# Optimization experiments

Measured on AMD Instinct MI355X. Metric: run time of the kernel, lower is better.

## Reference

```python
import jax, jax.numpy as jnp
import numpy as np

B, S, E, H = 32, 256, 768, 32
D = E // H  # head_dim = 24


def setup_inputs() -> dict:
    key = jax.random.key(0)
    ks = jax.random.split(key, 10)
    w_sc = 1.0 / np.sqrt(E)  # xavier-ish init scale for weights
    return {
        "feats": jax.random.normal(ks[0], (B, S, E), jnp.float32),
        "attn_bias": jax.random.normal(ks[1], (B, H, S, S), jnp.float32),
        "delta_pos": jax.random.normal(ks[2], (B, S, S, 3), jnp.float32),
        "Wq": jax.random.normal(ks[3], (E, E), jnp.float32) * w_sc,
        "bq": jnp.zeros((E,), jnp.float32),
        "Wk": jax.random.normal(ks[4], (E, E), jnp.float32) * w_sc,
        "bk": jnp.zeros((E,), jnp.float32),
        "Wv": jax.random.normal(ks[5], (E, E), jnp.float32) * w_sc,
        "bv": jnp.zeros((E,), jnp.float32),
        "Wfx": jax.random.normal(ks[6], (E,), jnp.float32) * w_sc,
        "Wfy": jax.random.normal(ks[7], (E,), jnp.float32) * w_sc,
        "Wfz": jax.random.normal(ks[8], (E,), jnp.float32) * w_sc,
    }


def reference(feats, attn_bias, delta_pos, Wq, bq, Wk, bk, Wv, bv, Wfx, Wfy, Wfz):
    b, s, e = feats.shape
    h = attn_bias.shape[1]
    d = e // h
    scaling = d ** -0.5
    # q/k/v projections; q scaled by 1/sqrt(head_dim)
    q = ((feats @ Wq + bq) * scaling).reshape(b, s, h, d).transpose(0, 2, 1, 3)  # (b,h,s,d)
    k = (feats @ Wk + bk).reshape(b, s, h, d).transpose(0, 2, 1, 3)              # (b,h,t,d)
    v = (feats @ Wv + bv).reshape(b, s, h, d).transpose(0, 2, 1, 3)              # (b,h,t,d)
    scores = jnp.einsum('bhsd,bhtd->bhst', q, k) + attn_bias
    probs = jax.nn.softmax(scores, axis=-1)  # dropout p in eval -> identity
    # rot_attn_probs = probs[...,None] * delta_pos[:,None] fused into one contraction:
    # (b,h,s,t) * (b,s,t,3) contracted with (b,h,t,c) over t -> (b,s,3,h,c)
    attn = jnp.einsum('bhst,bstx,bhtc->bsxhc', probs, delta_pos, v)
    attn = attn.reshape(b, s, 3, e)  # flatten (h,c) -> e
    out_x = attn[..., 0, :] @ Wfx  # (b,s)
    out_y = attn[..., 1, :] @ Wfy
    out_z = attn[..., 2, :] @ Wfz
    return jnp.stack([out_x, out_y, out_z], axis=-1)  # (b,s,3)
```

## Files before the change

### kernel.cpp

```cpp
#include <hip/hip_runtime.h>
#include <hip/hip_bf16.h>

#define B_ 32
#define S_ 256
#define E_ 768
#define H_ 32
#define D_ 24
#define NTOT 1664
#define LK 40

typedef __hip_bfloat16 bf16;
typedef __attribute__((ext_vector_type(8))) short short8;
typedef __attribute__((ext_vector_type(4))) float floatx4;

__global__ __launch_bounds__(256) void cast_feats(
    const float* __restrict__ in, bf16* __restrict__ outp, int n4)
{
  int i = blockIdx.x * 256 + threadIdx.x;
  if (i < n4) {
    float4 v = reinterpret_cast<const float4*>(in)[i];
    union { ushort4 u; bf16 b[4]; } pk;
    pk.b[0] = (bf16)v.x; pk.b[1] = (bf16)v.y;
    pk.b[2] = (bf16)v.z; pk.b[3] = (bf16)v.w;
    reinterpret_cast<ushort4*>(outp)[i] = pk.u;
  }
}

__global__ __launch_bounds__(256) void prep_pack(
    const float* __restrict__ Wq, const float* __restrict__ Wk,
    const float* __restrict__ Wv,
    const float* __restrict__ bq, const float* __restrict__ bk,
    const float* __restrict__ bv,
    const float* __restrict__ Wfx, const float* __restrict__ Wfy,
    const float* __restrict__ Wfz,
    bf16* __restrict__ Wt, float* __restrict__ biasf)
{
  const float qscale = 0.20412414523193154f;
  int gid = blockIdx.x * 256 + threadIdx.x;
  if (gid < NTOT * E_) {
    int n = gid / E_, k = gid % E_;
    float val;
    if (n < 768) {
      val = Wq[(size_t)k * E_ + n] * qscale;
    } else if (n < 1536) {
      val = Wk[(size_t)k * E_ + (n - 768)];
    } else if (n < 1632) {
      int nn = n - 1536, x = nn >> 5, h = nn & 31;
      const float* Wf = (x == 0) ? Wfx : (x == 1 ? Wfy : Wfz);
      float s = 0.f;
      #pragma unroll
      for (int c = 0; c < D_; c++)
        s += Wv[(size_t)k * E_ + h * D_ + c] * Wf[h * D_ + c];
      val = s;
    } else {
      val = 0.f;
    }
    Wt[gid] = (bf16)val;
  } else {
    int n = gid - NTOT * E_;
    if (n < NTOT) {
      float val;
      if (n < 768) {
        val = bq[n] * qscale;
      } else if (n < 1536) {
        val = bk[n - 768];
      } else if (n < 1632) {
        int nn = n - 1536, x = nn >> 5, h = nn & 31;
        const float* Wf = (x == 0) ? Wfx : (x == 1 ? Wfy : Wfz);
        float s = 0.f;
        #pragma unroll
        for (int c = 0; c < D_; c++)
          s += bv[h * D_ + c] * Wf[h * D_ + c];
        val = s;
      } else {
        val = 0.f;
      }
      biasf[n] = val;
    }
  }
}

__global__ __launch_bounds__(256) void gemm_qkv(
    const bf16* __restrict__ A, const bf16* __restrict__ Wt,
    const float* __restrict__ biasf,
    bf16* __restrict__ qout, bf16* __restrict__ kout,
    float* __restrict__ vwout)
{
  __shared__ __align__(16) short As[128 * LK];
  __shared__ __align__(16) short Bs[128 * LK];
  int tid = threadIdx.x;
  int m0 = blockIdx.y * 128, n0 = blockIdx.x * 128;
  int lrow = tid >> 2, lcol = (tid & 3) * 8;
  int wave = tid >> 6, lane = tid & 63;
  int wm = (wave >> 1) * 64, wn = (wave & 1) * 64;
  int fr = lane & 15, quad = lane >> 4;

  floatx4 acc[4][4];
  const floatx4 zero = {0.f, 0.f, 0.f, 0.f};
  #pragma unroll
  for (int i = 0; i < 4; i++)
    #pragma unroll
    for (int j = 0; j < 4; j++) acc[i][j] = zero;

  for (int k0 = 0; k0 < E_; k0 += 32) {
    float4 av0 = *reinterpret_cast<const float4*>(
        A + (size_t)(m0 + lrow) * E_ + k0 + lcol);
    float4 av1 = *reinterpret_cast<const float4*>(
        A + (size_t)(m0 + 64 + lrow) * E_ + k0 + lcol);
    float4 bv0 = *reinterpret_cast<const float4*>(
        Wt + (size_t)(n0 + lrow) * E_ + k0 + lcol);
    float4 bv1 = *reinterpret_cast<const float4*>(
        Wt + (size_t)(n0 + 64 + lrow) * E_ + k0 + lcol);
    __syncthreads();
    *reinterpret_cast<float4*>(&As[lrow * LK + lcol]) = av0;
    *reinterpret_cast<float4*>(&As[(lrow + 64) * LK + lcol]) = av1;
    *reinterpret_cast<float4*>(&Bs[lrow * LK + lcol]) = bv0;
    *reinterpret_cast<float4*>(&Bs[(lrow + 64) * LK + lcol]) = bv1;
    __syncthreads();
    short8 af[4], bfr[4];
    #pragma unroll
    for (int t = 0; t < 4; t++)
      af[t] = *reinterpret_cast<const short8*>(
          &As[(wm + t * 16 + fr) * LK + quad * 8]);
    #pragma unroll
    for (int t = 0; t < 4; t++)
      bfr[t] = *reinterpret_cast<const short8*>(
          &Bs[(wn + t * 16 + fr) * LK + quad * 8]);
    #pragma unroll
    for (int ti = 0; ti < 4; ti++)
      #pragma unroll
      for (int tj = 0; tj < 4; tj++)
        acc[ti][tj] = __builtin_amdgcn_mfma_f32_16x16x32_bf16(
            af[ti], bfr[tj], acc[ti][tj], 0, 0, 0);
  }

  #pragma unroll
  for (int ti = 0; ti < 4; ti++) {
    #pragma unroll
    for (int tj = 0; tj < 4; tj++) {
      int n = n0 + wn + tj * 16 + fr;
      float bias = biasf[n];
      #pragma unroll
      for (int r = 0; r < 4; r++) {
        int m = m0 + wm + ti * 16 + quad * 4 + r;
        int b = m >> 8, s = m & 255;
        float val = acc[ti][tj][r] + bias;
        if (n < 768) {
          int h = n / 24, d = n - h * 24;
          qout[(((size_t)b * H_ + h) * S_ + s) * D_ + d] = (bf16)val;
        } else if (n < 1536) {
          int n2 = n - 768;
          int h = n2 / 24, d = n2 - h * 24;
          kout[(((size_t)b * H_ + h) * S_ + s) * D_ + d] = (bf16)val;
        } else if (n < 1632) {
          int nn = n - 1536, x = nn >> 5, h = nn & 31;
          vwout[(((size_t)x * B_ + b) * H_ + h) * S_ + s] = val;
        }
      }
    }
  }
}

__global__ __launch_bounds__(256) void attn_kernel(
    const bf16* __restrict__ qg, const bf16* __restrict__ kg,
    const float* __restrict__ vwg, const float* __restrict__ biasg,
    const float* __restrict__ dpg, float* __restrict__ out)
{
  __shared__ float kl[S_ * 25];
  __shared__ float vwl[3][S_];
  int bh = blockIdx.x;
  int b = bh >> 5, h = bh & 31;
  int tid = threadIdx.x;
  {
    const bf16* krow = kg + ((size_t)bh * S_ + tid) * D_;
    #pragma unroll
    for (int d = 0; d < D_; d++) kl[tid * 25 + d] = (float)krow[d];
    #pragma unroll
    for (int x = 0; x < 3; x++)
      vwl[x][tid] = vwg[(((size_t)x * B_ + b) * H_ + h) * S_ + tid];
  }
  __syncthreads();

  int wave = tid >> 6, lane = tid & 63;
  const float* biasbh = biasg + (size_t)bh * S_ * S_;

  for (int s = wave; s < S_; s += 4) {
    const bf16* qrow = qg + ((size_t)bh * S_ + s) * D_;
    float qreg[D_];
    #pragma unroll
    for (int d = 0; d < D_; d++) qreg[d] = (float)qrow[d];

    float sc[4];
    #pragma unroll
    for (int j = 0; j < 4; j++) {
      int t = lane + 64 * j;
      float a = biasbh[s * S_ + t];
      #pragma unroll
      for (int d = 0; d < D_; d++) a += qreg[d] * kl[t * 25 + d];
      sc[j] = a;
    }
    float mx = fmaxf(fmaxf(sc[0], sc[1]), fmaxf(sc[2], sc[3]));
    #pragma unroll
    for (int o = 32; o; o >>= 1) mx = fmaxf(mx, __shfl_xor(mx, o));
    float p[4], l = 0.f;
    #pragma unroll
    for (int j = 0; j < 4; j++) { p[j] = __expf(sc[j] - mx); l += p[j]; }
    #pragma unroll
    for (int o = 32; o; o >>= 1) l += __shfl_xor(l, o);
    float inv = 1.0f / l;

    float ax = 0.f, ay = 0.f, az = 0.f;
    const float* dprow = dpg + ((size_t)(b * S_ + s) * S_) * 3;
    #pragma unroll
    for (int j = 0; j < 4; j++) {
      int t = lane + 64 * j;
      float w = p[j] * inv;
      float3 dp3 = *reinterpret_cast<const float3*>(&dprow[t * 3]);
      ax += w * dp3.x * vwl[0][t];
      ay += w * dp3.y * vwl[1][t];
      az += w * dp3.z * vwl[2][t];
    }
    #pragma unroll
    for (int o = 32; o; o >>= 1) {
      ax += __shfl_xor(ax, o);
      ay += __shfl_xor(ay, o);
      az += __shfl_xor(az, o);
    }
    if (lane == 0) {
      float* op = out + (size_t)(b * S_ + s) * 3;
      atomicAdd(op + 0, ax);
      atomicAdd(op + 1, ay);
      atomicAdd(op + 2, az);
    }
  }
}

extern "C" void kernel_launch(void* const* d_in, const int* in_sizes, int n_in,
                              void* d_out, int out_size, void* d_ws, size_t ws_size,
                              hipStream_t stream)
{
  const float* feats     = (const float*)d_in[0];
  const float* attn_bias = (const float*)d_in[1];
  const float* delta_pos = (const float*)d_in[2];
  const float* Wq        = (const float*)d_in[3];
  const float* bq        = (const float*)d_in[4];
  const float* Wk        = (const float*)d_in[5];
  const float* bk        = (const float*)d_in[6];
  const float* Wv        = (const float*)d_in[7];
  const float* bv        = (const float*)d_in[8];
  const float* Wfx       = (const float*)d_in[9];
  const float* Wfy       = (const float*)d_in[10];
  const float* Wfz       = (const float*)d_in[11];

  char* ws = (char*)d_ws;
  size_t off = 0;
  auto alloc = [&](size_t bytes) -> void* {
    void* p = ws + off;
    off = (off + bytes + 255) & ~(size_t)255;
    return p;
  };
  bf16*  ws_fb   = (bf16*) alloc((size_t)B_ * S_ * E_ * 2);
  bf16*  ws_q    = (bf16*) alloc((size_t)B_ * H_ * S_ * D_ * 2);
  bf16*  ws_k    = (bf16*) alloc((size_t)B_ * H_ * S_ * D_ * 2);
  float* ws_vw   = (float*)alloc((size_t)3 * B_ * H_ * S_ * 4);
  bf16*  ws_Wt   = (bf16*) alloc((size_t)NTOT * E_ * 2);
  float* ws_bias = (float*)alloc((size_t)NTOT * 4);

  hipMemsetAsync(d_out, 0, (size_t)B_ * S_ * 3 * 4, stream);

  int n4 = B_ * S_ * E_ / 4;
  cast_feats<<<(n4 + 255) / 256, 256, 0, stream>>>(feats, ws_fb, n4);

  int prep_n = NTOT * E_ + NTOT;
  prep_pack<<<(prep_n + 255) / 256, 256, 0, stream>>>(
      Wq, Wk, Wv, bq, bk, bv, Wfx, Wfy, Wfz, ws_Wt, ws_bias);

  gemm_qkv<<<dim3(NTOT / 128, B_ * S_ / 128), 256, 0, stream>>>(
      ws_fb, ws_Wt, ws_bias, ws_q, ws_k, ws_vw);

  attn_kernel<<<B_ * H_, 256, 0, stream>>>(ws_q, ws_k, ws_vw, attn_bias,
                                           delta_pos, (float*)d_out);
}
```

Before: 656.0 us.

## Register-resident K tiles and split attention into four query blocks; prefetch GEMM tiles

The attention kernel now launches four blocks per (batch, head), each handling 64 query rows. Each lane keeps four contiguous key rows and their vw weights in registers, and uses packed float2 FMAs for the dot products. Bias and delta_pos are read with vectorized float4 loads over contiguous t, and Q is staged in shared memory. The QKV GEMM also register-prefetches the next K-slice of global tiles before the MFMA work. The aim is more parallelism and occupancy plus coalesced streaming of the large bias and delta_pos tensors, at the cost of higher register pressure and K/vw being reloaded four times.

```diff
diff --git a/kernel.cpp b/kernel.cpp
--- a/kernel.cpp
+++ b/kernel.cpp
@@ -12,6 +12,7 @@
 typedef __hip_bfloat16 bf16;
 typedef __attribute__((ext_vector_type(8))) short short8;
 typedef __attribute__((ext_vector_type(4))) float floatx4;
+typedef __attribute__((ext_vector_type(2))) float f32x2;
 
 __global__ __launch_bounds__(256) void cast_feats(
     const float* __restrict__ in, bf16* __restrict__ outp, int n4)
@@ -102,21 +103,26 @@
     #pragma unroll
     for (int j = 0; j < 4; j++) acc[i][j] = zero;
 
+  const bf16* Aptr = A + (size_t)(m0 + lrow) * E_ + lcol;
+  const bf16* Bptr = Wt + (size_t)(n0 + lrow) * E_ + lcol;
+  float4 av0 = *reinterpret_cast<const float4*>(Aptr);
+  float4 av1 = *reinterpret_cast<const float4*>(Aptr + (size_t)64 * E_);
+  float4 bv0 = *reinterpret_cast<const float4*>(Bptr);
+  float4 bv1 = *reinterpret_cast<const float4*>(Bptr + (size_t)64 * E_);
+
   for (int k0 = 0; k0 < E_; k0 += 32) {
-    float4 av0 = *reinterpret_cast<const float4*>(
-        A + (size_t)(m0 + lrow) * E_ + k0 + lcol);
-    float4 av1 = *reinterpret_cast<const float4*>(
-        A + (size_t)(m0 + 64 + lrow) * E_ + k0 + lcol);
-    float4 bv0 = *reinterpret_cast<const float4*>(
-        Wt + (size_t)(n0 + lrow) * E_ + k0 + lcol);
-    float4 bv1 = *reinterpret_cast<const float4*>(
-        Wt + (size_t)(n0 + 64 + lrow) * E_ + k0 + lcol);
     __syncthreads();
     *reinterpret_cast<float4*>(&As[lrow * LK + lcol]) = av0;
     *reinterpret_cast<float4*>(&As[(lrow + 64) * LK + lcol]) = av1;
     *reinterpret_cast<float4*>(&Bs[lrow * LK + lcol]) = bv0;
     *reinterpret_cast<float4*>(&Bs[(lrow + 64) * LK + lcol]) = bv1;
     __syncthreads();
+    if (k0 + 32 < E_) {
+      av0 = *reinterpret_cast<const float4*>(Aptr + k0 + 32);
+      av1 = *reinterpret_cast<const float4*>(Aptr + (size_t)64 * E_ + k0 + 32);
+      bv0 = *reinterpret_cast<const float4*>(Bptr + k0 + 32);
+      bv1 = *reinterpret_cast<const float4*>(Bptr + (size_t)64 * E_ + k0 + 32);
+    }
     short8 af[4], bfr[4];
     #pragma unroll
     for (int t = 0; t < 4; t++)
@@ -161,44 +167,71 @@
   }
 }
 
-__global__ __launch_bounds__(256) void attn_kernel(
+__global__ __launch_bounds__(256, 3) void attn_kernel(
     const bf16* __restrict__ qg, const bf16* __restrict__ kg,
     const float* __restrict__ vwg, const float* __restrict__ biasg,
     const float* __restrict__ dpg, float* __restrict__ out)
 {
-  __shared__ float kl[S_ * 25];
-  __shared__ float vwl[3][S_];
-  int bh = blockIdx.x;
+  __shared__ float ql[64 * 26];
+  int blk = blockIdx.x;
+  int bh = blk >> 2, st = (blk & 3) * 64;
   int b = bh >> 5, h = bh & 31;
-  int tid = threadIdx.x;
+  int tid = threadIdx.x, wave = tid >> 6, lane = tid & 63;
+  int t0 = lane * 4;
+
+  f32x2 kr[4][12];
+  #pragma unroll
+  for (int j = 0; j < 4; j++) {
+    const bf16* krow = kg + ((size_t)bh * S_ + t0 + j) * D_;
+    #pragma unroll
+    for (int i = 0; i < 12; i++) {
+      f32x2 kk;
+      kk.x = (float)krow[2 * i];
+      kk.y = (float)krow[2 * i + 1];
+      kr[j][i] = kk;
+    }
+  }
+  float vwr[3][4];
+  #pragma unroll
+  for (int x = 0; x < 3; x++) {
+    float4 v4 = *reinterpret_cast<const float4*>(
+        vwg + (((size_t)x * B_ + b) * H_ + h) * S_ + t0);
+    vwr[x][0] = v4.x; vwr[x][1] = v4.y; vwr[x][2] = v4.z; vwr[x][3] = v4.w;
+  }
   {
-    const bf16* krow = kg + ((size_t)bh * S_ + tid) * D_;
-    #pragma unroll
-    for (int d = 0; d < D_; d++) kl[tid * 25 + d] = (float)krow[d];
-    #pragma unroll
-    for (int x = 0; x < 3; x++)
-      vwl[x][tid] = vwg[(((size_t)x * B_ + b) * H_ + h) * S_ + tid];
+    int r = tid >> 2, c0 = (tid & 3) * 6;
+    const bf16* qrow = qg + ((size_t)bh * S_ + st + r) * D_ + c0;
+    #pragma unroll
+    for (int i = 0; i < 6; i++) ql[r * 26 + c0 + i] = (float)qrow[i];
   }
   __syncthreads();
 
-  int wave = tid >> 6, lane = tid & 63;
   const float* biasbh = biasg + (size_t)bh * S_ * S_;
 
-  for (int s = wave; s < S_; s += 4) {
-    const bf16* qrow = qg + ((size_t)bh * S_ + s) * D_;
-    float qreg[D_];
-    #pragma unroll
-    for (int d = 0; d < D_; d++) qreg[d] = (float)qrow[d];
-
+  for (int si = 0; si < 16; si++) {
+    int sr = si * 4 + wave;
+    int s = st + sr;
+    float4 bias4 = *reinterpret_cast<const float4*>(biasbh + s * S_ + t0);
+    const float* dpr = dpg + ((size_t)(b * S_ + s) * S_) * 3 + (size_t)t0 * 3;
+    float4 d0 = *reinterpret_cast<const float4*>(dpr);
+    float4 d1 = *reinterpret_cast<const float4*>(dpr + 4);
+    float4 d2 = *reinterpret_cast<const float4*>(dpr + 8);
+
+    f32x2 sc2[4];
+    #pragma unroll
+    for (int j = 0; j < 4; j++) { sc2[j].x = 0.f; sc2[j].y = 0.f; }
+    #pragma unroll
+    for (int i = 0; i < 12; i++) {
+      f32x2 qd = *reinterpret_cast<const f32x2*>(&ql[sr * 26 + 2 * i]);
+      #pragma unroll
+      for (int j = 0; j < 4; j++) sc2[j] += qd * kr[j][i];
+    }
     float sc[4];
-    #pragma unroll
-    for (int j = 0; j < 4; j++) {
-      int t = lane + 64 * j;
-      float a = biasbh[s * S_ + t];
-      #pragma unroll
-      for (int d = 0; d < D_; d++) a += qreg[d] * kl[t * 25 + d];
-      sc[j] = a;
-    }
+    sc[0] = sc2[0].x + sc2[0].y + bias4.x;
+    sc[1] = sc2[1].x + sc2[1].y + bias4.y;
+    sc[2] = sc2[2].x + sc2[2].y + bias4.z;
+    sc[3] = sc2[3].x + sc2[3].y + bias4.w;
+
     float mx = fmaxf(fmaxf(sc[0], sc[1]), fmaxf(sc[2], sc[3]));
     #pragma unroll
     for (int o = 32; o; o >>= 1) mx = fmaxf(mx, __shfl_xor(mx, o));
@@ -209,16 +242,17 @@
     for (int o = 32; o; o >>= 1) l += __shfl_xor(l, o);
     float inv = 1.0f / l;
 
+    float dx[4] = {d0.x, d0.w, d1.z, d2.y};
+    float dy[4] = {d0.y, d1.x, d1.w, d2.z};
+    float dz[4] = {d0.z, d1.y, d2.x, d2.w};
+
     float ax = 0.f, ay = 0.f, az = 0.f;
-    const float* dprow = dpg + ((size_t)(b * S_ + s) * S_) * 3;
     #pragma unroll
     for (int j = 0; j < 4; j++) {
-      int t = lane + 64 * j;
       float w = p[j] * inv;
-      float3 dp3 = *reinterpret_cast<const float3*>(&dprow[t * 3]);
-      ax += w * dp3.x * vwl[0][t];
-      ay += w * dp3.y * vwl[1][t];
-      az += w * dp3.z * vwl[2][t];
+      ax += w * dx[j] * vwr[0][j];
+      ay += w * dy[j] * vwr[1][j];
+      az += w * dz[j] * vwr[2][j];
     }
     #pragma unroll
     for (int o = 32; o; o >>= 1) {
@@ -278,6 +312,6 @@
   gemm_qkv<<<dim3(NTOT / 128, B_ * S_ / 128), 256, 0, stream>>>(
       ws_fb, ws_Wt, ws_bias, ws_q, ws_k, ws_vw);
 
-  attn_kernel<<<B_ * H_, 256, 0, stream>>>(ws_q, ws_k, ws_vw, attn_bias,
-                                           delta_pos, (float*)d_out);
-}
+  attn_kernel<<<B_ * H_ * 4, 256, 0, stream>>>(ws_q, ws_k, ws_vw, attn_bias,
+                                               delta_pos, (float*)d_out);
+}
```

Measured after the change: 608.4 us. 1.08x faster.

## Use MFMA for attention scores, tile weight transpose, prefetch GEMM tiles

Applied to the files above, without the earlier changes.

The attention kernel now computes QK^T with bf16 16x16x32 MFMA instructions from zero-padded Q/K tiles in LDS, replacing scalar dot products. It also drops the softmax max subtraction and normalizes each row once at the end. Weight preparation is split into an LDS-tiled transpose of Wq/Wk plus a small kernel for the folded V weights and biases, replacing a strided-read transpose. The QKV GEMM prefetches the next K-slice into registers while the current slice computes. The costs are per-lane bias and delta_pos reads with a less coalesced pattern, and possible exp overflow when scores are large.

```diff
diff --git a/kernel.cpp b/kernel.cpp
--- a/kernel.cpp
+++ b/kernel.cpp
@@ -26,38 +26,58 @@
   }
 }
 
-__global__ __launch_bounds__(256) void prep_pack(
+__global__ __launch_bounds__(256) void transpose_w(
     const float* __restrict__ Wq, const float* __restrict__ Wk,
-    const float* __restrict__ Wv,
+    bf16* __restrict__ Wt)
+{
+  __shared__ float tile[64][65];
+  int z = blockIdx.z;
+  const float* src = z ? Wk : Wq;
+  float scale = z ? 1.0f : 0.20412414523193154f;
+  int k0 = blockIdx.x * 64, n0 = blockIdx.y * 64;
+  int tid = threadIdx.x;
+  int rr = tid >> 4, cc = (tid & 15) * 4;
+  #pragma unroll
+  for (int i = 0; i < 4; i++) {
+    float4 v = *reinterpret_cast<const float4*>(
+        &src[(size_t)(k0 + rr + i * 16) * E_ + n0 + cc]);
+    tile[rr + i * 16][cc + 0] = v.x;
+    tile[rr + i * 16][cc + 1] = v.y;
+    tile[rr + i * 16][cc + 2] = v.z;
+    tile[rr + i * 16][cc + 3] = v.w;
+  }
+  __syncthreads();
+  #pragma unroll
+  for (int i = 0; i < 4; i++) {
+    int n = rr + i * 16;
+    union { ushort4 u; bf16 h[4]; } pk;
+    #pragma unroll
+    for (int j = 0; j < 4; j++) pk.h[j] = (bf16)(tile[cc + j][n] * scale);
+    *reinterpret_cast<ushort4*>(
+        &Wt[(size_t)(z * 768 + n0 + n) * E_ + k0 + cc]) = pk.u;
+  }
+}
+
+__global__ __launch_bounds__(256) void prep_vwx(
+    const float* __restrict__ Wv, const float* __restrict__ bv,
     const float* __restrict__ bq, const float* __restrict__ bk,
-    const float* __restrict__ bv,
     const float* __restrict__ Wfx, const float* __restrict__ Wfy,
     const float* __restrict__ Wfz,
     bf16* __restrict__ Wt, float* __restrict__ biasf)
 {
   const float qscale = 0.20412414523193154f;
   int gid = blockIdx.x * 256 + threadIdx.x;
-  if (gid < NTOT * E_) {
-    int n = gid / E_, k = gid % E_;
-    float val;
-    if (n < 768) {
-      val = Wq[(size_t)k * E_ + n] * qscale;
-    } else if (n < 1536) {
-      val = Wk[(size_t)k * E_ + (n - 768)];
-    } else if (n < 1632) {
-      int nn = n - 1536, x = nn >> 5, h = nn & 31;
-      const float* Wf = (x == 0) ? Wfx : (x == 1 ? Wfy : Wfz);
-      float s = 0.f;
-      #pragma unroll
-      for (int c = 0; c < D_; c++)
-        s += Wv[(size_t)k * E_ + h * D_ + c] * Wf[h * D_ + c];
-      val = s;
-    } else {
-      val = 0.f;
-    }
-    Wt[gid] = (bf16)val;
+  if (gid < 96 * E_) {
+    int k = gid / 96, nn = gid % 96;
+    int x = nn >> 5, h = nn & 31;
+    const float* Wf = (x == 0) ? Wfx : (x == 1 ? Wfy : Wfz);
+    float s = 0.f;
+    #pragma unroll
+    for (int c = 0; c < D_; c++)
+      s += Wv[(size_t)k * E_ + h * D_ + c] * Wf[h * D_ + c];
+    Wt[(size_t)(1536 + nn) * E_ + k] = (bf16)s;
   } else {
-    int n = gid - NTOT * E_;
+    int n = gid - 96 * E_;
     if (n < NTOT) {
       float val;
       if (n < 768) {
@@ -102,21 +122,26 @@
     #pragma unroll
     for (int j = 0; j < 4; j++) acc[i][j] = zero;
 
+  const bf16* Aptr = A + (size_t)(m0 + lrow) * E_ + lcol;
+  const bf16* Bptr = Wt + (size_t)(n0 + lrow) * E_ + lcol;
+  float4 av0 = *reinterpret_cast<const float4*>(Aptr);
+  float4 av1 = *reinterpret_cast<const float4*>(Aptr + (size_t)64 * E_);
+  float4 bv0 = *reinterpret_cast<const float4*>(Bptr);
+  float4 bv1 = *reinterpret_cast<const float4*>(Bptr + (size_t)64 * E_);
+
   for (int k0 = 0; k0 < E_; k0 += 32) {
-    float4 av0 = *reinterpret_cast<const float4*>(
-        A + (size_t)(m0 + lrow) * E_ + k0 + lcol);
-    float4 av1 = *reinterpret_cast<const float4*>(
-        A + (size_t)(m0 + 64 + lrow) * E_ + k0 + lcol);
-    float4 bv0 = *reinterpret_cast<const float4*>(
-        Wt + (size_t)(n0 + lrow) * E_ + k0 + lcol);
-    float4 bv1 = *reinterpret_cast<const float4*>(
-        Wt + (size_t)(n0 + 64 + lrow) * E_ + k0 + lcol);
     __syncthreads();
     *reinterpret_cast<float4*>(&As[lrow * LK + lcol]) = av0;
     *reinterpret_cast<float4*>(&As[(lrow + 64) * LK + lcol]) = av1;
     *reinterpret_cast<float4*>(&Bs[lrow * LK + lcol]) = bv0;
     *reinterpret_cast<float4*>(&Bs[(lrow + 64) * LK + lcol]) = bv1;
     __syncthreads();
+    if (k0 + 32 < E_) {
+      av0 = *reinterpret_cast<const float4*>(Aptr + k0 + 32);
+      av1 = *reinterpret_cast<const float4*>(Aptr + (size_t)64 * E_ + k0 + 32);
+      bv0 = *reinterpret_cast<const float4*>(Bptr + k0 + 32);
+      bv1 = *reinterpret_cast<const float4*>(Bptr + (size_t)64 * E_ + k0 + 32);
+    }
     short8 af[4], bfr[4];
     #pragma unroll
     for (int t = 0; t < 4; t++)
@@ -161,76 +186,92 @@
   }
 }
 
-__global__ __launch_bounds__(256) void attn_kernel(
+__global__ __launch_bounds__(256, 4) void attn_kernel(
     const bf16* __restrict__ qg, const bf16* __restrict__ kg,
     const float* __restrict__ vwg, const float* __restrict__ biasg,
     const float* __restrict__ dpg, float* __restrict__ out)
 {
-  __shared__ float kl[S_ * 25];
-  __shared__ float vwl[3][S_];
+  __shared__ __align__(16) short qs[S_ * 32];
+  __shared__ __align__(16) short ks[S_ * 32];
+  __shared__ float vwl[3 * S_];
   int bh = blockIdx.x;
   int b = bh >> 5, h = bh & 31;
   int tid = threadIdx.x;
+
   {
-    const bf16* krow = kg + ((size_t)bh * S_ + tid) * D_;
-    #pragma unroll
-    for (int d = 0; d < D_; d++) kl[tid * 25 + d] = (float)krow[d];
+    const float4* qrow = reinterpret_cast<const float4*>(
+        qg + ((size_t)bh * S_ + tid) * D_);
+    const float4* krow = reinterpret_cast<const float4*>(
+        kg + ((size_t)bh * S_ + tid) * D_);
+    float4 zz = {0.f, 0.f, 0.f, 0.f};
+    *reinterpret_cast<float4*>(&qs[tid * 32 + 0])  = qrow[0];
+    *reinterpret_cast<float4*>(&qs[tid * 32 + 8])  = qrow[1];
+    *reinterpret_cast<float4*>(&qs[tid * 32 + 16]) = qrow[2];
+    *reinterpret_cast<float4*>(&qs[tid * 32 + 24]) = zz;
+    *reinterpret_cast<float4*>(&ks[tid * 32 + 0])  = krow[0];
+    *reinterpret_cast<float4*>(&ks[tid * 32 + 8])  = krow[1];
+    *reinterpret_cast<float4*>(&ks[tid * 32 + 16]) = krow[2];
+    *reinterpret_cast<float4*>(&ks[tid * 32 + 24]) = zz;
     #pragma unroll
     for (int x = 0; x < 3; x++)
-      vwl[x][tid] = vwg[(((size_t)x * B_ + b) * H_ + h) * S_ + tid];
+      vwl[x * S_ + tid] = vwg[(((size_t)x * B_ + b) * H_ + h) * S_ + tid];
   }
   __syncthreads();
 
   int wave = tid >> 6, lane = tid & 63;
+  int fr = lane & 15, quad = lane >> 4;
   const float* biasbh = biasg + (size_t)bh * S_ * S_;
-
-  for (int s = wave; s < S_; s += 4) {
-    const bf16* qrow = qg + ((size_t)bh * S_ + s) * D_;
-    float qreg[D_];
-    #pragma unroll
-    for (int d = 0; d < D_; d++) qreg[d] = (float)qrow[d];
-
-    float sc[4];
-    #pragma unroll
-    for (int j = 0; j < 4; j++) {
-      int t = lane + 64 * j;
-      float a = biasbh[s * S_ + t];
-      #pragma unroll
-      for (int d = 0; d < D_; d++) a += qreg[d] * kl[t * 25 + d];
-      sc[j] = a;
-    }
-    float mx = fmaxf(fmaxf(sc[0], sc[1]), fmaxf(sc[2], sc[3]));
-    #pragma unroll
-    for (int o = 32; o; o >>= 1) mx = fmaxf(mx, __shfl_xor(mx, o));
-    float p[4], l = 0.f;
-    #pragma unroll
-    for (int j = 0; j < 4; j++) { p[j] = __expf(sc[j] - mx); l += p[j]; }
-    #pragma unroll
-    for (int o = 32; o; o >>= 1) l += __shfl_xor(l, o);
-    float inv = 1.0f / l;
-
-    float ax = 0.f, ay = 0.f, az = 0.f;
-    const float* dprow = dpg + ((size_t)(b * S_ + s) * S_) * 3;
-    #pragma unroll
-    for (int j = 0; j < 4; j++) {
-      int t = lane + 64 * j;
-      float w = p[j] * inv;
-      float3 dp3 = *reinterpret_cast<const float3*>(&dprow[t * 3]);
-      ax += w * dp3.x * vwl[0][t];
-      ay += w * dp3.y * vwl[1][t];
-      az += w * dp3.z * vwl[2][t];
-    }
-    #pragma unroll
-    for (int o = 32; o; o >>= 1) {
-      ax += __shfl_xor(ax, o);
-      ay += __shfl_xor(ay, o);
-      az += __shfl_xor(az, o);
-    }
-    if (lane == 0) {
-      float* op = out + (size_t)(b * S_ + s) * 3;
-      atomicAdd(op + 0, ax);
-      atomicAdd(op + 1, ay);
-      atomicAdd(op + 2, az);
+  const floatx4 zero = {0.f, 0.f, 0.f, 0.f};
+
+  for (int it = 0; it < 4; it++) {
+    int s0 = it * 64 + wave * 16;
+    short8 afrag = *reinterpret_cast<const short8*>(
+        &qs[(s0 + fr) * 32 + quad * 8]);
+    float l[4] = {0.f, 0.f, 0.f, 0.f};
+    float ax[4] = {0.f, 0.f, 0.f, 0.f};
+    float ay[4] = {0.f, 0.f, 0.f, 0.f};
+    float az[4] = {0.f, 0.f, 0.f, 0.f};
+
+    #pragma unroll
+    for (int tt = 0; tt < 16; tt++) {
+      short8 bfrag = *reinterpret_cast<const short8*>(
+          &ks[(tt * 16 + fr) * 32 + quad * 8]);
+      floatx4 c = __builtin_amdgcn_mfma_f32_16x16x32_bf16(
+          afrag, bfrag, zero, 0, 0, 0);
+      int t = tt * 16 + fr;
+      float vx = vwl[t], vy = vwl[S_ + t], vz = vwl[2 * S_ + t];
+      #pragma unroll
+      for (int r = 0; r < 4; r++) {
+        int s = s0 + quad * 4 + r;
+        float e = __expf(c[r] + biasbh[(size_t)s * S_ + t]);
+        const float* dp = dpg + ((size_t)(b * S_ + s) * S_ + t) * 3;
+        l[r] += e;
+        ax[r] += e * dp[0] * vx;
+        ay[r] += e * dp[1] * vy;
+        az[r] += e * dp[2] * vz;
+      }
+    }
+
+    #pragma unroll
+    for (int o = 1; o < 16; o <<= 1) {
+      #pragma unroll
+      for (int r = 0; r < 4; r++) {
+        l[r]  += __shfl_xor(l[r], o);
+        ax[r] += __shfl_xor(ax[r], o);
+        ay[r] += __shfl_xor(ay[r], o);
+        az[r] += __shfl_xor(az[r], o);
+      }
+    }
+    if (fr == 0) {
+      #pragma unroll
+      for (int r = 0; r < 4; r++) {
+        int s = s0 + quad * 4 + r;
+        float inv = 1.0f / l[r];
+        float* op = out + (size_t)(b * S_ + s) * 3;
+        atomicAdd(op + 0, ax[r] * inv);
+        atomicAdd(op + 1, ay[r] * inv);
+        atomicAdd(op + 2, az[r] * inv);
+      }
     }
   }
 }
@@ -271,9 +312,11 @@
   int n4 = B_ * S_ * E_ / 4;
   cast_feats<<<(n4 + 255) / 256, 256, 0, stream>>>(feats, ws_fb, n4);
 
-  int prep_n = NTOT * E_ + NTOT;
-  prep_pack<<<(prep_n + 255) / 256, 256, 0, stream>>>(
-      Wq, Wk, Wv, bq, bk, bv, Wfx, Wfy, Wfz, ws_Wt, ws_bias);
+  transpose_w<<<dim3(12, 12, 2), 256, 0, stream>>>(Wq, Wk, ws_Wt);
+
+  int prep_n = 96 * E_ + NTOT;
+  prep_vwx<<<(prep_n + 255) / 256, 256, 0, stream>>>(
+      Wv, bv, bq, bk, Wfx, Wfy, Wfz, ws_Wt, ws_bias);
 
   gemm_qkv<<<dim3(NTOT / 128, B_ * S_ / 128), 256, 0, stream>>>(
       ws_fb, ws_Wt, ws_bias, ws_q, ws_k, ws_vw);
```

Measured after the change: 760.4 us. 1.16x slower.
